# Kernel tuning notes

Measured on AMD Instinct MI355X. Metric: run time of the kernel, lower is better.

Reference implementation:

```python
import jax, jax.numpy as jnp
import numpy as np

B, S, D_IN = 2, 2048, 2048
H, G, HD = 16, 4, 128          # heads, kv groups, head_dim
GS = H // G                    # group size (heads per kv group)
EPS = 1e-6
SCALE = HD ** -0.5


def rms_norm(x, w):
    # RMSNorm over last dim (head_dim)
    var = jnp.mean(jnp.square(x), axis=-1, keepdims=True)
    return x * jax.lax.rsqrt(var + EPS) * w


def apply_rope(x, cos, sin):
    # x: [b, h, s, d]; cos/sin: [s, d]. Rotate-half convention.
    d = x.shape[-1]
    x1, x2 = x[..., : d // 2], x[..., d // 2 :]
    rotated = jnp.concatenate([-x2, x1], axis=-1)
    return x * cos[None, None] + rotated * sin[None, None]


def setup_inputs() -> dict:
    key = jax.random.key(0)
    ks = jax.random.split(key, 8)
    x = jax.random.normal(ks[0], (B, S, D_IN), jnp.float32)
    mask = jnp.triu(jnp.ones((S, S), jnp.bool_), k=1)  # True = masked (future)
    # realistic RoPE tables
    inv_freq = 1.0 / (10000.0 ** (jnp.arange(0, HD, 2, dtype=jnp.float32) / HD))
    angles = jnp.arange(S, dtype=jnp.float32)[:, None] * inv_freq[None, :]  # [S, HD/2]
    angles = jnp.concatenate([angles, angles], axis=-1)  # [S, HD]
    cos, sin = jnp.cos(angles), jnp.sin(angles)
    sd = 0.02
    Wq = jax.random.normal(ks[1], (D_IN, H * HD), jnp.float32) * sd
    Wk = jax.random.normal(ks[2], (D_IN, G * HD), jnp.float32) * sd
    Wv = jax.random.normal(ks[3], (D_IN, G * HD), jnp.float32) * sd
    Wo = jax.random.normal(ks[4], (H * HD, D_IN), jnp.float32) * sd
    q_norm_w = jnp.ones((HD,), jnp.float32)
    k_norm_w = jnp.ones((HD,), jnp.float32)
    return {"x": x, "mask": mask, "cos": cos, "sin": sin, "Wq": Wq, "Wk": Wk,
            "Wv": Wv, "Wo": Wo, "q_norm_w": q_norm_w, "k_norm_w": k_norm_w}


def reference(x, mask, cos, sin, Wq, Wk, Wv, Wo, q_norm_w, k_norm_w):
    b, s, _ = x.shape
    q = (x @ Wq).reshape(b, s, H, HD).transpose(0, 2, 1, 3)   # [b,H,s,d]
    k = (x @ Wk).reshape(b, s, G, HD).transpose(0, 2, 1, 3)   # [b,G,s,d]
    v = (x @ Wv).reshape(b, s, G, HD).transpose(0, 2, 1, 3)   # [b,G,s,d]
    q = rms_norm(q, q_norm_w)
    k = rms_norm(k, k_norm_w)
    q = apply_rope(q, cos, sin)
    k = apply_rope(k, cos, sin)
    q = q * SCALE
    # GQA without materializing repeated KV: split heads into [G, GS]
    qg = q.reshape(b, G, GS, s, HD)                           # [b,G,gs,s,d]
    scores = jnp.einsum('bghsd,bgtd->bghst', qg, k)           # [b,G,gs,s,s]
    scores = jnp.where(mask[None, None, None], -jnp.inf, scores)
    attn = jax.nn.softmax(scores, axis=-1)
    ctx = jnp.einsum('bghst,bgtd->bghsd', attn, v)            # [b,G,gs,s,d]
    ctx = ctx.reshape(b, H, s, HD).transpose(0, 2, 1, 3).reshape(b, s, H * HD)
    return ctx @ Wo
```

## Files before the change

kernel.cpp:

```cpp
#include <hip/hip_runtime.h>
#include <cstdint>
#include <cstddef>

typedef unsigned short u16;
typedef __bf16 bf16x8 __attribute__((ext_vector_type(8)));
typedef float f32x4 __attribute__((ext_vector_type(4)));

#define SLEN 2048
#define NHEADS 16
#define NGRP 4

__device__ inline float bf2f(u16 u) { return __uint_as_float(((unsigned)u) << 16); }
__device__ inline u16 f2bf(float f) {
    unsigned u = __float_as_uint(f);
    u += 0x7fffu + ((u >> 16) & 1u);
    return (u16)(u >> 16);
}

__device__ inline f32x4 mfma16(bf16x8 a, bf16x8 b, f32x4 c) {
    return __builtin_amdgcn_mfma_f32_16x16x32_bf16(a, b, c, 0, 0, 0);
}

__device__ inline void memfence_compiler() { __asm__ volatile("" ::: "memory"); }

__device__ inline void cp16(const u16* g, u16* l) {
    __builtin_amdgcn_global_load_lds(
        (__attribute__((address_space(1))) void*)(u16*)g,
        (__attribute__((address_space(3))) void*)l, 16, 0, 0);
}


__device__ inline void transpose_f32_body(u16 (*tile)[65], const float* __restrict__ in,
                                          u16* __restrict__ out, int R, int C, int bx, int by,
                                          int tid) {
    const long r0 = (long)by * 64, c0 = (long)bx * 64;
    for (int j = 0; j < 4; j++) {
        int c = j * 256 + tid;
        int lr = c >> 4, lc = (c & 15) * 4;
        float4 v = *(const float4*)&in[(r0 + lr) * (long)C + c0 + lc];
        tile[lr][lc + 0] = f2bf(v.x); tile[lr][lc + 1] = f2bf(v.y);
        tile[lr][lc + 2] = f2bf(v.z); tile[lr][lc + 3] = f2bf(v.w);
    }
    __syncthreads();
    for (int j = 0; j < 4; j++) {
        int c = j * 256 + tid;
        int orow = c >> 4, oc = (c & 15) * 4;
        ushort4 vv;
        vv.x = tile[oc + 0][orow]; vv.y = tile[oc + 1][orow];
        vv.z = tile[oc + 2][orow]; vv.w = tile[oc + 3][orow];
        *(ushort4*)&out[(c0 + orow) * (long)R + r0 + oc] = vv;
    }
}

__device__ inline void transpose_bf_body(u16 (*tile)[65], const u16* __restrict__ in, long inRS,
                                         u16* __restrict__ out, int R, int C, int bx, int by,
                                         int tid) {
    const long r0 = (long)by * 64, c0 = (long)bx * 64;
    for (int j = 0; j < 4; j++) {
        int c = j * 256 + tid;
        int lr = c >> 4, lc = (c & 15) * 4;
        ushort4 vv = *(const ushort4*)&in[(r0 + lr) * inRS + c0 + lc];
        tile[lr][lc + 0] = vv.x; tile[lr][lc + 1] = vv.y;
        tile[lr][lc + 2] = vv.z; tile[lr][lc + 3] = vv.w;
    }
    __syncthreads();
    for (int j = 0; j < 4; j++) {
        int c = j * 256 + tid;
        int orow = c >> 4, oc = (c & 15) * 4;
        ushort4 vv;
        vv.x = tile[oc + 0][orow]; vv.y = tile[oc + 1][orow];
        vv.z = tile[oc + 2][orow]; vv.w = tile[oc + 3][orow];
        *(ushort4*)&out[(c0 + orow) * (long)R + r0 + oc] = vv;
    }
}

__device__ inline void normrope_body(u16* __restrict__ buf, long rowstride, int heads,
                                     const u16* __restrict__ w,
                                     const float* __restrict__ cosf, const float* __restrict__ sinf,
                                     float scale, int row, int lane) {
    u16* p = buf + (long)(row / heads) * rowstride + (row % heads) * 128;
    float x1 = bf2f(p[lane]);
    float x2 = bf2f(p[lane + 64]);
    float ss = x1 * x1 + x2 * x2;
    for (int off = 1; off < 64; off <<= 1) ss += __shfl_xor(ss, off);
    float inv = rsqrtf(ss * (1.f / 128.f) + 1e-6f);
    int s = (row / heads) % SLEN;
    float c1 = cosf[s * 128 + lane], c2 = cosf[s * 128 + 64 + lane];
    float s1 = sinf[s * 128 + lane], s2 = sinf[s * 128 + 64 + lane];
    float w1 = bf2f(w[lane]), w2 = bf2f(w[lane + 64]);
    float y1 = x1 * inv * w1, y2 = x2 * inv * w2;
    p[lane]      = f2bf((y1 * c1 - y2 * s1) * scale);
    p[lane + 64] = f2bf((y2 * c2 + y1 * s2) * scale);
}

__global__ __launch_bounds__(256) void prep_k(const float* __restrict__ x, u16* __restrict__ xbf,
                                              const float* __restrict__ qw, const float* __restrict__ kw,
                                              u16* qwb, u16* kwb,
                                              const float* __restrict__ Wq, const float* __restrict__ Wk,
                                              const float* __restrict__ Wv, u16* __restrict__ wqkvT) {
    __shared__ u16 tile[64][65];
    const int bid = blockIdx.x, tid = threadIdx.x;
    if (bid < 8192) {
        long i = ((long)bid * 256 + tid) * 4;
        float4 v = *(const float4*)(x + i);
        ushort4 o;
        o.x = f2bf(v.x); o.y = f2bf(v.y); o.z = f2bf(v.z); o.w = f2bf(v.w);
        *(ushort4*)(xbf + i) = o;
    } else if (bid == 8192) {
        if (tid < 128) qwb[tid] = f2bf(qw[tid]);
        else kwb[tid - 128] = f2bf(kw[tid - 128]);
    } else if (bid < 9217) {
        int rem = bid - 8193;
        transpose_f32_body(tile, Wq, wqkvT, 2048, 2048, rem & 31, rem >> 5, tid);
    } else if (bid < 9473) {
        int rem = bid - 9217;
        transpose_f32_body(tile, Wk, wqkvT + 2048L * 2048, 2048, 512, rem & 7, rem >> 3, tid);
    } else {
        int rem = bid - 9473;
        transpose_f32_body(tile, Wv, wqkvT + 2560L * 2048, 2048, 512, rem & 7, rem >> 3, tid);
    }
}

__global__ __launch_bounds__(256) void mid_k(u16* __restrict__ qkvb, u16* __restrict__ vTb,
                                             const u16* __restrict__ qwb, const u16* __restrict__ kwb,
                                             const float* __restrict__ cosf, const float* __restrict__ sinf,
                                             const float* __restrict__ Wo, u16* __restrict__ woT) {
    __shared__ u16 tile[64][65];
    const int bid = blockIdx.x, tid = threadIdx.x;
    if (bid < 512) {
        transpose_bf_body(tile, qkvb + 2560, 3072L, vTb, 4096, 512, bid & 7, bid >> 3, tid);
    } else if (bid < 16896) {
        int row = (bid - 512) * 4 + (tid >> 6);
        normrope_body(qkvb, 3072L, NHEADS, qwb, cosf, sinf, 0.08838834764831845f, row, tid & 63);
    } else if (bid < 20992) {
        int row = (bid - 16896) * 4 + (tid >> 6);
        normrope_body(qkvb + 2048, 3072L, NGRP, kwb, cosf, sinf, 1.0f, row, tid & 63);
    } else {
        int rem = bid - 20992;
        transpose_f32_body(tile, Wo, woT, 2048, 2048, rem & 31, rem >> 5, tid);
    }
}

template <typename OutT, int NI>
__global__ __launch_bounds__(512, 2) void gemm8p(const u16* __restrict__ A, const u16* __restrict__ Bt,
                                                 OutT* __restrict__ C, int N, int K) {
    extern __shared__ u16 smem[];
    constexpr int AUNIT = 8192;
    constexpr int BUNIT = NI * 2048;
    constexpr int GATE = 2 + NI / 2;
    const int tid = threadIdx.x;
    const int lane = tid & 63, wave = tid >> 6;
    const int l15 = lane & 15, quad = lane >> 4;
    const int wm = (wave >> 2) * 128, wn = (wave & 3) * (NI * 16);
    const long m0 = (long)blockIdx.y * 256, n0 = (long)blockIdx.x * (NI * 64);

    f32x4 acc[8][NI];
    #pragma unroll
    for (int i = 0; i < 8; i++)
        #pragma unroll
        for (int j = 0; j < NI; j++) acc[i][j] = {0.f, 0.f, 0.f, 0.f};

    const u16* aBase = A + m0 * (long)K;
    const u16* bBase = Bt + n0 * (long)K;

    auto stageA = [&](int kt, int c, int k) {
        u16* dst = smem + (c * 2 + k) * AUNIT + wave * 512;
        #pragma unroll
        for (int i = 0; i < 2; i++) {
            int cd = i * 512 + wave * 64 + lane;
            int r = cd >> 2;
            int js = (cd & 3) ^ ((r >> 1) & 3);
            cp16(aBase + (long)r * K + kt + k * 32 + js * 8, dst + i * 4096);
        }
    };
    auto stageB = [&](int kt, int c, int k) {
        u16* dst = smem + 4 * AUNIT + (c * 2 + k) * BUNIT + wave * 512;
        #pragma unroll
        for (int i = 0; i < NI / 2; i++) {
            int cd = i * 512 + wave * 64 + lane;
            int r = cd >> 2;
            int js = (cd & 3) ^ ((r >> 1) & 3);
            cp16(bBase + (long)r * K + kt + k * 32 + js * 8, dst + i * 4096);
        }
    };

    stageA(0, 0, 0); stageB(0, 0, 0); stageA(0, 0, 1); stageB(0, 0, 1);

    const int nkt = K >> 6;

    for (int t = 0; t < nkt; ++t) {
        const int c = t & 1;
        const int kt1 = (t + 1) << 6;
        const bool more = (t + 1) < nkt;
        #pragma unroll
        for (int k = 0; k < 2; ++k) {
            if (k == 0 || more) {
                if constexpr (NI == 4) asm volatile("s_waitcnt vmcnt(4)" ::: "memory");
                else                   asm volatile("s_waitcnt vmcnt(3)" ::: "memory");
            } else {
                asm volatile("s_waitcnt vmcnt(0)" ::: "memory");
            }
            __builtin_amdgcn_s_barrier();

            const u16* au = smem + (c * 2 + k) * AUNIT;
            const u16* bu = smem + 4 * AUNIT + (c * 2 + k) * BUNIT;

            bf16x8 bfr[NI], af[4];
            #pragma unroll
            for (int ni = 0; ni < NI; ni++) {
                const int r = wn + ni * 16 + l15;
                bfr[ni] = *(const bf16x8*)&bu[r * 32 + (quad ^ ((r >> 1) & 3)) * 8];
            }
            #pragma unroll
            for (int mi = 0; mi < 4; mi++) {
                const int r = wm + mi * 16 + l15;
                af[mi] = *(const bf16x8*)&au[r * 32 + (quad ^ ((r >> 1) & 3)) * 8];
            }
            if (more) stageA(kt1, c ^ 1, k);
            asm volatile("s_waitcnt lgkmcnt(0)" ::: "memory");
            __builtin_amdgcn_sched_barrier(0);
            __builtin_amdgcn_s_setprio(1);
            #pragma unroll
            for (int mi = 0; mi < 4; mi++)
                #pragma unroll
                for (int ni = 0; ni < NI; ni++)
                    acc[mi][ni] = mfma16(af[mi], bfr[ni], acc[mi][ni]);
            __builtin_amdgcn_s_setprio(0);
            __builtin_amdgcn_s_barrier();

            #pragma unroll
            for (int mi = 0; mi < 4; mi++) {
                const int r = wm + 64 + mi * 16 + l15;
                af[mi] = *(const bf16x8*)&au[r * 32 + (quad ^ ((r >> 1) & 3)) * 8];
            }
            if (more) stageB(kt1, c ^ 1, k);
            asm volatile("s_waitcnt lgkmcnt(0)" ::: "memory");
            __builtin_amdgcn_sched_barrier(0);
            __builtin_amdgcn_s_setprio(1);
            #pragma unroll
            for (int mi = 0; mi < 4; mi++)
                #pragma unroll
                for (int ni = 0; ni < NI; ni++)
                    acc[4 + mi][ni] = mfma16(af[mi], bfr[ni], acc[4 + mi][ni]);
            __builtin_amdgcn_s_setprio(0);
            __builtin_amdgcn_s_barrier();
        }
    }

    #pragma unroll
    for (int mi = 0; mi < 8; mi++)
        #pragma unroll
        for (int r = 0; r < 4; r++) {
            long row = m0 + wm + mi * 16 + quad * 4 + r;
            OutT* crow = C + row * (long)N + n0 + wn + l15;
            #pragma unroll
            for (int ni = 0; ni < NI; ni++) {
                float v = acc[mi][ni][r];
                if constexpr (sizeof(OutT) == 2) crow[ni * 16] = f2bf(v);
                else crow[ni * 16] = v;
            }
        }
}

__global__ __launch_bounds__(256, 2) void attn(const u16* __restrict__ qkv, const u16* __restrict__ vT,
                                               u16* __restrict__ ctx) {
    __shared__ u16 KB[64 * 128];
    __shared__ u16 VB[128 * 64];
    __shared__ u16 Ps[4][2][16][72];
    __shared__ float Al[4][2][16];
    const int tid = threadIdx.x;
    const int lane = tid & 63, wave = tid >> 6;
    const int l15 = lane & 15, quad = lane >> 4;
    const int bg = blockIdx.x & 7, b = bg >> 2, g = bg & 3;
    const int rest = blockIdx.x >> 3;
    const int h = g * 4 + (rest & 3);
    const int idx = rest >> 2;
    const int qt = (idx < 8) ? (15 - idx) : (idx - 8);
    const int wr = qt * 128 + wave * 32;

    union { bf16x8 v; u16 s[8]; } uo;
    for (int j = 0; j < 8; j++) uo.s[j] = 0x3F80;
    const bf16x8 ones = uo.v;

    bf16x8 qa[2][4];
    for (int m = 0; m < 2; m++) {
        const u16* qp = qkv + (long)(b * SLEN + wr + m * 16 + l15) * 3072 + h * 128 + quad * 8;
        for (int kc = 0; kc < 4; kc++) qa[m][kc] = *(const bf16x8*)(qp + kc * 32);
    }
    float m_i[2] = {-__builtin_inff(), -__builtin_inff()};
    f32x4 l_acc[2];
    f32x4 o[2][8];
    for (int m = 0; m < 2; m++) l_acc[m] = {0.f, 0.f, 0.f, 0.f};
    for (int m = 0; m < 2; m++)
        for (int nf = 0; nf < 8; nf++) o[m][nf] = {0.f, 0.f, 0.f, 0.f};

    const u16* kqb = qkv + (long)b * SLEN * 3072 + 2048 + g * 128;
    const u16* vgb = vT + (long)g * 128 * 4096 + (long)b * SLEN;
    const int xk = (l15 & 7) << 4;
    const int nt = 2 * qt + 2;

    for (int t = 0; t < nt; ++t) {
        const int t0 = t * 64;
        #pragma unroll
        for (int i = 0; i < 4; ++i) {
            const int j = wave * 4 + i;
            {
                const int row = j * 4 + (lane >> 4);
                const int cs = lane & 15;
                cp16(kqb + (long)(t0 + row) * 3072 + ((cs ^ (row & 7)) * 8), &KB[j * 512]);
            }
            {
                const int row = j * 8 + (lane >> 3);
                const int cs = lane & 7;
                cp16(vgb + (long)row * 4096 + t0 + ((cs ^ (row & 7)) * 8), &VB[j * 512]);
            }
        }
        __syncthreads();

        if (t0 <= wr + 31) {
            bf16x8 kf[4][4];
            #pragma unroll
            for (int nf = 0; nf < 4; nf++)
                #pragma unroll
                for (int kc = 0; kc < 4; kc++)
                    kf[nf][kc] = *(const bf16x8*)((const char*)KB +
                                  (nf * 16 + l15) * 256 + ((quad * 16 + kc * 64) ^ xk));

            f32x4 sc[2][4];
            for (int m = 0; m < 2; m++)
                for (int nf = 0; nf < 4; nf++) sc[m][nf] = {0.f, 0.f, 0.f, 0.f};
            #pragma unroll
            for (int kc = 0; kc < 4; kc++)
                #pragma unroll
                for (int nf = 0; nf < 4; nf++) {
                    sc[0][nf] = mfma16(kf[nf][kc], qa[0][kc], sc[0][nf]);
                    sc[1][nf] = mfma16(kf[nf][kc], qa[1][kc], sc[1][nf]);
                }
            if (t0 + 63 > wr) {
                #pragma unroll
                for (int m = 0; m < 2; m++) {
                    int qrow = wr + m * 16 + l15;
                    #pragma unroll
                    for (int nf = 0; nf < 4; nf++)
                        #pragma unroll
                        for (int r = 0; r < 4; r++)
                            if (t0 + nf * 16 + quad * 4 + r > qrow) sc[m][nf][r] = -__builtin_inff();
                }
            }
            float alpha[2];
            #pragma unroll
            for (int m = 0; m < 2; m++) {
                float mx = sc[m][0][0];
                #pragma unroll
                for (int nf = 0; nf < 4; nf++)
                    #pragma unroll
                    for (int r = 0; r < 4; r++) mx = fmaxf(mx, sc[m][nf][r]);
                mx = fmaxf(mx, __shfl_xor(mx, 16));
                mx = fmaxf(mx, __shfl_xor(mx, 32));
                float mn = fmaxf(m_i[m], mx);
                alpha[m] = __expf(m_i[m] - mn);
                m_i[m] = mn;
                Al[wave][m][l15] = alpha[m];
            }
            #pragma unroll
            for (int m = 0; m < 2; m++)
                #pragma unroll
                for (int nf = 0; nf < 4; nf++) {
                    ushort4 pk;
                    pk.x = f2bf(__expf(sc[m][nf][0] - m_i[m]));
                    pk.y = f2bf(__expf(sc[m][nf][1] - m_i[m]));
                    pk.z = f2bf(__expf(sc[m][nf][2] - m_i[m]));
                    pk.w = f2bf(__expf(sc[m][nf][3] - m_i[m]));
                    *(ushort4*)&Ps[wave][m][l15][nf * 16 + quad * 4] = pk;
                }
            memfence_compiler();
            f32x4 al[2];
            al[0] = *(const f32x4*)&Al[wave][0][quad * 4];
            al[1] = *(const f32x4*)&Al[wave][1][quad * 4];
            #pragma unroll
            for (int m = 0; m < 2; m++) {
                #pragma unroll
                for (int nf = 0; nf < 8; nf++)
                    #pragma unroll
                    for (int r = 0; r < 4; r++) o[m][nf][r] *= al[m][r];
                #pragma unroll
                for (int r = 0; r < 4; r++) l_acc[m][r] *= al[m][r];
            }
            {
                bf16x8 vf[8];
                #pragma unroll
                for (int nf = 0; nf < 8; nf++)
                    vf[nf] = *(const bf16x8*)((const char*)VB +
                              (nf * 16 + l15) * 128 + ((quad * 16) ^ xk));
                bf16x8 pa0 = *(const bf16x8*)&Ps[wave][0][l15][quad * 8];
                bf16x8 pa1 = *(const bf16x8*)&Ps[wave][1][l15][quad * 8];
                #pragma unroll
                for (int nf = 0; nf < 8; nf++) {
                    o[0][nf] = mfma16(pa0, vf[nf], o[0][nf]);
                    o[1][nf] = mfma16(pa1, vf[nf], o[1][nf]);
                }
                l_acc[0] = mfma16(pa0, ones, l_acc[0]);
                l_acc[1] = mfma16(pa1, ones, l_acc[1]);
            }
            {
                bf16x8 vf[8];
                #pragma unroll
                for (int nf = 0; nf < 8; nf++)
                    vf[nf] = *(const bf16x8*)((const char*)VB +
                              (nf * 16 + l15) * 128 + ((64 + quad * 16) ^ xk));
                bf16x8 pa0 = *(const bf16x8*)&Ps[wave][0][l15][32 + quad * 8];
                bf16x8 pa1 = *(const bf16x8*)&Ps[wave][1][l15][32 + quad * 8];
                #pragma unroll
                for (int nf = 0; nf < 8; nf++) {
                    o[0][nf] = mfma16(pa0, vf[nf], o[0][nf]);
                    o[1][nf] = mfma16(pa1, vf[nf], o[1][nf]);
                }
                l_acc[0] = mfma16(pa0, ones, l_acc[0]);
                l_acc[1] = mfma16(pa1, ones, l_acc[1]);
            }
            memfence_compiler();
        }
        __syncthreads();
    }

    #pragma unroll
    for (int m = 0; m < 2; m++)
        #pragma unroll
        for (int r = 0; r < 4; r++) {
            float inv = 1.f / l_acc[m][r];
            int srow = wr + m * 16 + quad * 4 + r;
            u16* cp = ctx + (long)(b * SLEN + srow) * 2048 + h * 128 + l15;
            #pragma unroll
            for (int nf = 0; nf < 8; nf++) cp[nf * 16] = f2bf(o[m][nf][r] * inv);
        }
}

extern "C" void kernel_launch(void* const* d_in, const int* in_sizes, int n_in,
                              void* d_out, int out_size, void* d_ws, size_t ws_size,
                              hipStream_t stream) {
    const float* x    = (const float*)d_in[0];
    const float* cosi = (const float*)d_in[2];
    const float* sini = (const float*)d_in[3];
    const float* Wq   = (const float*)d_in[4];
    const float* Wk   = (const float*)d_in[5];
    const float* Wv   = (const float*)d_in[6];
    const float* Wo   = (const float*)d_in[7];
    const float* qw   = (const float*)d_in[8];
    const float* kw   = (const float*)d_in[9];
    float* out = (float*)d_out;
    char* ws = (char*)d_ws;

    const size_t MB = 1 << 20;
    u16* qkvb  = (u16*)(ws);
    u16* vTb   = (u16*)(ws + 24 * MB);
    u16* xbf   = (u16*)(ws + 28 * MB);
    u16* ctx   = (u16*)(ws + 28 * MB);
    u16* wqkvT = (u16*)(ws + 44 * MB);
    u16* woT   = (u16*)(ws + 44 * MB);
    u16* qwb   = (u16*)(ws + 56 * MB);
    u16* kwb   = (u16*)(ws + 56 * MB + 256);

    prep_k<<<9729, 256, 0, stream>>>(x, xbf, qw, kw, qwb, kwb, Wq, Wk, Wv, wqkvT);

    gemm8p<u16, 4><<<dim3(12, 16), 512, 131072, stream>>>(xbf, wqkvT, qkvb, 3072, 2048);

    mid_k<<<22016, 256, 0, stream>>>(qkvb, vTb, qwb, kwb, cosi, sini, Wo, woT);

    attn<<<dim3(512, 1, 1), 256, 0, stream>>>(qkvb, vTb, ctx);

    gemm8p<float, 2><<<dim3(16, 16), 512, 98304, stream>>>(ctx, woT, out, 2048, 2048);
}
```

Baseline: 320.2 us.

## Double-buffer attention K/V tiles, hoist V fragments, swizzle GEMM block order

The attention kernel now double-buffers the K and V shared tiles. It prefetches the next tile with async copies while computing on the current one, and uses a partial vmcnt wait instead of a full sync. V fragments are loaded once per tile, and the P staging buffer is cut to one row-block per wave, reused across the two m iterations. In the GEMM, both A fragment halves are loaded up front with a partial lgkmcnt wait, and block indices are remapped in an XCD-aware interleave to improve L2 locality. The changes cost more LDS and registers, which may hurt occupancy, and they rely on exact async-copy counts and per-wave buffer reuse being ordered correctly.

```diff
diff --git a/kernel.cpp b/kernel.cpp
--- a/kernel.cpp
+++ b/kernel.cpp
@@ -147,12 +147,16 @@
     extern __shared__ u16 smem[];
     constexpr int AUNIT = 8192;
     constexpr int BUNIT = NI * 2048;
-    constexpr int GATE = 2 + NI / 2;
     const int tid = threadIdx.x;
     const int lane = tid & 63, wave = tid >> 6;
     const int l15 = lane & 15, quad = lane >> 4;
     const int wm = (wave >> 2) * 128, wn = (wave & 3) * (NI * 16);
-    const long m0 = (long)blockIdx.y * 256, n0 = (long)blockIdx.x * (NI * 64);
+
+    const int nbx = gridDim.x;
+    const int nwg = nbx * gridDim.y;
+    const int d = blockIdx.y * nbx + blockIdx.x;
+    const int s = (d & 7) * (nwg >> 3) + (d >> 3);
+    const long m0 = (long)(s / nbx) * 256, n0 = (long)(s % nbx) * (NI * 64);
 
     f32x4 acc[8][NI];
     #pragma unroll
@@ -205,7 +209,7 @@
             const u16* au = smem + (c * 2 + k) * AUNIT;
             const u16* bu = smem + 4 * AUNIT + (c * 2 + k) * BUNIT;
 
-            bf16x8 bfr[NI], af[4];
+            bf16x8 bfr[NI], af0[4], af1[4];
             #pragma unroll
             for (int ni = 0; ni < NI; ni++) {
                 const int r = wn + ni * 16 + l15;
@@ -214,25 +218,25 @@
             #pragma unroll
             for (int mi = 0; mi < 4; mi++) {
                 const int r = wm + mi * 16 + l15;
-                af[mi] = *(const bf16x8*)&au[r * 32 + (quad ^ ((r >> 1) & 3)) * 8];
+                af0[mi] = *(const bf16x8*)&au[r * 32 + (quad ^ ((r >> 1) & 3)) * 8];
+            }
+            #pragma unroll
+            for (int mi = 0; mi < 4; mi++) {
+                const int r = wm + 64 + mi * 16 + l15;
+                af1[mi] = *(const bf16x8*)&au[r * 32 + (quad ^ ((r >> 1) & 3)) * 8];
             }
             if (more) stageA(kt1, c ^ 1, k);
-            asm volatile("s_waitcnt lgkmcnt(0)" ::: "memory");
+            asm volatile("s_waitcnt lgkmcnt(4)" ::: "memory");
             __builtin_amdgcn_sched_barrier(0);
             __builtin_amdgcn_s_setprio(1);
             #pragma unroll
             for (int mi = 0; mi < 4; mi++)
                 #pragma unroll
                 for (int ni = 0; ni < NI; ni++)
-                    acc[mi][ni] = mfma16(af[mi], bfr[ni], acc[mi][ni]);
+                    acc[mi][ni] = mfma16(af0[mi], bfr[ni], acc[mi][ni]);
             __builtin_amdgcn_s_setprio(0);
             __builtin_amdgcn_s_barrier();
 
-            #pragma unroll
-            for (int mi = 0; mi < 4; mi++) {
-                const int r = wm + 64 + mi * 16 + l15;
-                af[mi] = *(const bf16x8*)&au[r * 32 + (quad ^ ((r >> 1) & 3)) * 8];
-            }
             if (more) stageB(kt1, c ^ 1, k);
             asm volatile("s_waitcnt lgkmcnt(0)" ::: "memory");
             __builtin_amdgcn_sched_barrier(0);
@@ -241,7 +245,7 @@
             for (int mi = 0; mi < 4; mi++)
                 #pragma unroll
                 for (int ni = 0; ni < NI; ni++)
-                    acc[4 + mi][ni] = mfma16(af[mi], bfr[ni], acc[4 + mi][ni]);
+                    acc[4 + mi][ni] = mfma16(af1[mi], bfr[ni], acc[4 + mi][ni]);
             __builtin_amdgcn_s_setprio(0);
             __builtin_amdgcn_s_barrier();
         }
@@ -264,9 +268,9 @@
 
 __global__ __launch_bounds__(256, 2) void attn(const u16* __restrict__ qkv, const u16* __restrict__ vT,
                                                u16* __restrict__ ctx) {
-    __shared__ u16 KB[64 * 128];
-    __shared__ u16 VB[128 * 64];
-    __shared__ u16 Ps[4][2][16][72];
+    __shared__ u16 KB[2][64 * 128];
+    __shared__ u16 VB[2][128 * 64];
+    __shared__ u16 Ps[4][16][72];
     __shared__ float Al[4][2][16];
     const int tid = threadIdx.x;
     const int lane = tid & 63, wave = tid >> 6;
@@ -299,23 +303,35 @@
     const int xk = (l15 & 7) << 4;
     const int nt = 2 * qt + 2;
 
-    for (int t = 0; t < nt; ++t) {
-        const int t0 = t * 64;
+    auto stage = [&](int t0, int buf) {
         #pragma unroll
         for (int i = 0; i < 4; ++i) {
             const int j = wave * 4 + i;
             {
                 const int row = j * 4 + (lane >> 4);
                 const int cs = lane & 15;
-                cp16(kqb + (long)(t0 + row) * 3072 + ((cs ^ (row & 7)) * 8), &KB[j * 512]);
+                cp16(kqb + (long)(t0 + row) * 3072 + ((cs ^ (row & 7)) * 8), &KB[buf][j * 512]);
             }
             {
                 const int row = j * 8 + (lane >> 3);
                 const int cs = lane & 7;
-                cp16(vgb + (long)row * 4096 + t0 + ((cs ^ (row & 7)) * 8), &VB[j * 512]);
-            }
-        }
-        __syncthreads();
+                cp16(vgb + (long)row * 4096 + t0 + ((cs ^ (row & 7)) * 8), &VB[buf][j * 512]);
+            }
+        }
+    };
+
+    stage(0, 0);
+
+    for (int t = 0; t < nt; ++t) {
+        const int cur = t & 1;
+        const int t0 = t * 64;
+        if (t + 1 < nt) {
+            stage((t + 1) * 64, cur ^ 1);
+            asm volatile("s_waitcnt vmcnt(8)" ::: "memory");
+        } else {
+            asm volatile("s_waitcnt vmcnt(0)" ::: "memory");
+        }
+        __builtin_amdgcn_s_barrier();
 
         if (t0 <= wr + 31) {
             bf16x8 kf[4][4];
@@ -323,7 +339,7 @@
             for (int nf = 0; nf < 4; nf++)
                 #pragma unroll
                 for (int kc = 0; kc < 4; kc++)
-                    kf[nf][kc] = *(const bf16x8*)((const char*)KB +
+                    kf[nf][kc] = *(const bf16x8*)((const char*)&KB[cur][0] +
                                   (nf * 16 + l15) * 256 + ((quad * 16 + kc * 64) ^ xk));
 
             f32x4 sc[2][4];
@@ -362,8 +378,22 @@
                 m_i[m] = mn;
                 Al[wave][m][l15] = alpha[m];
             }
-            #pragma unroll
-            for (int m = 0; m < 2; m++)
+            memfence_compiler();
+            f32x4 al[2];
+            al[0] = *(const f32x4*)&Al[wave][0][quad * 4];
+            al[1] = *(const f32x4*)&Al[wave][1][quad * 4];
+
+            bf16x8 vfA[8], vfB[8];
+            #pragma unroll
+            for (int nf = 0; nf < 8; nf++) {
+                vfA[nf] = *(const bf16x8*)((const char*)&VB[cur][0] +
+                          (nf * 16 + l15) * 128 + ((quad * 16) ^ xk));
+                vfB[nf] = *(const bf16x8*)((const char*)&VB[cur][0] +
+                          (nf * 16 + l15) * 128 + ((64 + quad * 16) ^ xk));
+            }
+
+            #pragma unroll
+            for (int m = 0; m < 2; m++) {
                 #pragma unroll
                 for (int nf = 0; nf < 4; nf++) {
                     ushort4 pk;
@@ -371,56 +401,29 @@
                     pk.y = f2bf(__expf(sc[m][nf][1] - m_i[m]));
                     pk.z = f2bf(__expf(sc[m][nf][2] - m_i[m]));
                     pk.w = f2bf(__expf(sc[m][nf][3] - m_i[m]));
-                    *(ushort4*)&Ps[wave][m][l15][nf * 16 + quad * 4] = pk;
+                    *(ushort4*)&Ps[wave][l15][nf * 16 + quad * 4] = pk;
                 }
-            memfence_compiler();
-            f32x4 al[2];
-            al[0] = *(const f32x4*)&Al[wave][0][quad * 4];
-            al[1] = *(const f32x4*)&Al[wave][1][quad * 4];
-            #pragma unroll
-            for (int m = 0; m < 2; m++) {
+                memfence_compiler();
                 #pragma unroll
                 for (int nf = 0; nf < 8; nf++)
                     #pragma unroll
                     for (int r = 0; r < 4; r++) o[m][nf][r] *= al[m][r];
                 #pragma unroll
                 for (int r = 0; r < 4; r++) l_acc[m][r] *= al[m][r];
-            }
-            {
-                bf16x8 vf[8];
-                #pragma unroll
-                for (int nf = 0; nf < 8; nf++)
-                    vf[nf] = *(const bf16x8*)((const char*)VB +
-                              (nf * 16 + l15) * 128 + ((quad * 16) ^ xk));
-                bf16x8 pa0 = *(const bf16x8*)&Ps[wave][0][l15][quad * 8];
-                bf16x8 pa1 = *(const bf16x8*)&Ps[wave][1][l15][quad * 8];
+                bf16x8 pa0 = *(const bf16x8*)&Ps[wave][l15][quad * 8];
+                bf16x8 pa1 = *(const bf16x8*)&Ps[wave][l15][32 + quad * 8];
                 #pragma unroll
                 for (int nf = 0; nf < 8; nf++) {
-                    o[0][nf] = mfma16(pa0, vf[nf], o[0][nf]);
-                    o[1][nf] = mfma16(pa1, vf[nf], o[1][nf]);
+                    o[m][nf] = mfma16(pa0, vfA[nf], o[m][nf]);
+                    o[m][nf] = mfma16(pa1, vfB[nf], o[m][nf]);
                 }
-                l_acc[0] = mfma16(pa0, ones, l_acc[0]);
-                l_acc[1] = mfma16(pa1, ones, l_acc[1]);
-            }
-            {
-                bf16x8 vf[8];
-                #pragma unroll
-                for (int nf = 0; nf < 8; nf++)
-                    vf[nf] = *(const bf16x8*)((const char*)VB +
-                              (nf * 16 + l15) * 128 + ((64 + quad * 16) ^ xk));
-                bf16x8 pa0 = *(const bf16x8*)&Ps[wave][0][l15][32 + quad * 8];
-                bf16x8 pa1 = *(const bf16x8*)&Ps[wave][1][l15][32 + quad * 8];
-                #pragma unroll
-                for (int nf = 0; nf < 8; nf++) {
-                    o[0][nf] = mfma16(pa0, vf[nf], o[0][nf]);
-                    o[1][nf] = mfma16(pa1, vf[nf], o[1][nf]);
-                }
-                l_acc[0] = mfma16(pa0, ones, l_acc[0]);
-                l_acc[1] = mfma16(pa1, ones, l_acc[1]);
-            }
-            memfence_compiler();
-        }
-        __syncthreads();
+                l_acc[m] = mfma16(pa0, ones, l_acc[m]);
+                l_acc[m] = mfma16(pa1, ones, l_acc[m]);
+                memfence_compiler();
+            }
+        }
+        memfence_compiler();
+        __builtin_amdgcn_s_barrier();
     }
 
     #pragma unroll
```

Result: no change. 315.0 us (-1.6%).

## Split long causal attention tiles across blocks with flag-synchronized merge, remap GEMM blocks

Applied to the files above, without the earlier changes.

The attention kernel now uses a static schedule table. Each block handles up to two query tiles, and the longest query tiles are split across two blocks by KV range. The block that owns the first half writes its partial output plus row max and row sum, then raises a flag; the second block spin-waits on that flag and merges the two halves using log-sum-exp rescaling. The aim is to balance the causal triangle's uneven work across the 512 blocks. Separately, the GEMM remaps block IDs across groups of 8 for better cache locality and loads both A-fragment halves before the first MFMA batch. The spin-wait relies on the producer block being resident or already finished, which risks deadlock or stalls if scheduling order differs.

```diff
diff --git a/kernel.cpp b/kernel.cpp
--- a/kernel.cpp
+++ b/kernel.cpp
@@ -124,7 +124,8 @@
 __global__ __launch_bounds__(256) void mid_k(u16* __restrict__ qkvb, u16* __restrict__ vTb,
                                              const u16* __restrict__ qwb, const u16* __restrict__ kwb,
                                              const float* __restrict__ cosf, const float* __restrict__ sinf,
-                                             const float* __restrict__ Wo, u16* __restrict__ woT) {
+                                             const float* __restrict__ Wo, u16* __restrict__ woT,
+                                             unsigned* __restrict__ flags) {
     __shared__ u16 tile[64][65];
     const int bid = blockIdx.x, tid = threadIdx.x;
     if (bid < 512) {
@@ -135,9 +136,11 @@
     } else if (bid < 20992) {
         int row = (bid - 16896) * 4 + (tid >> 6);
         normrope_body(qkvb + 2048, 3072L, NGRP, kwb, cosf, sinf, 1.0f, row, tid & 63);
-    } else {
+    } else if (bid < 22016) {
         int rem = bid - 20992;
         transpose_f32_body(tile, Wo, woT, 2048, 2048, rem & 31, rem >> 5, tid);
+    } else {
+        flags[tid] = 0u;
     }
 }
 
@@ -147,12 +150,16 @@
     extern __shared__ u16 smem[];
     constexpr int AUNIT = 8192;
     constexpr int BUNIT = NI * 2048;
-    constexpr int GATE = 2 + NI / 2;
     const int tid = threadIdx.x;
     const int lane = tid & 63, wave = tid >> 6;
     const int l15 = lane & 15, quad = lane >> 4;
     const int wm = (wave >> 2) * 128, wn = (wave & 3) * (NI * 16);
-    const long m0 = (long)blockIdx.y * 256, n0 = (long)blockIdx.x * (NI * 64);
+
+    const int nbx = gridDim.x;
+    const int nwg = nbx * gridDim.y;
+    const int d = blockIdx.y * nbx + blockIdx.x;
+    const int s = (d & 7) * (nwg >> 3) + (d >> 3);
+    const long m0 = (long)(s / nbx) * 256, n0 = (long)(s % nbx) * (NI * 64);
 
     f32x4 acc[8][NI];
     #pragma unroll
@@ -205,7 +212,7 @@
             const u16* au = smem + (c * 2 + k) * AUNIT;
             const u16* bu = smem + 4 * AUNIT + (c * 2 + k) * BUNIT;
 
-            bf16x8 bfr[NI], af[4];
+            bf16x8 bfr[NI], af0[4], af1[4];
             #pragma unroll
             for (int ni = 0; ni < NI; ni++) {
                 const int r = wn + ni * 16 + l15;
@@ -214,25 +221,25 @@
             #pragma unroll
             for (int mi = 0; mi < 4; mi++) {
                 const int r = wm + mi * 16 + l15;
-                af[mi] = *(const bf16x8*)&au[r * 32 + (quad ^ ((r >> 1) & 3)) * 8];
+                af0[mi] = *(const bf16x8*)&au[r * 32 + (quad ^ ((r >> 1) & 3)) * 8];
+            }
+            #pragma unroll
+            for (int mi = 0; mi < 4; mi++) {
+                const int r = wm + 64 + mi * 16 + l15;
+                af1[mi] = *(const bf16x8*)&au[r * 32 + (quad ^ ((r >> 1) & 3)) * 8];
             }
             if (more) stageA(kt1, c ^ 1, k);
-            asm volatile("s_waitcnt lgkmcnt(0)" ::: "memory");
+            asm volatile("s_waitcnt lgkmcnt(4)" ::: "memory");
             __builtin_amdgcn_sched_barrier(0);
             __builtin_amdgcn_s_setprio(1);
             #pragma unroll
             for (int mi = 0; mi < 4; mi++)
                 #pragma unroll
                 for (int ni = 0; ni < NI; ni++)
-                    acc[mi][ni] = mfma16(af[mi], bfr[ni], acc[mi][ni]);
+                    acc[mi][ni] = mfma16(af0[mi], bfr[ni], acc[mi][ni]);
             __builtin_amdgcn_s_setprio(0);
             __builtin_amdgcn_s_barrier();
 
-            #pragma unroll
-            for (int mi = 0; mi < 4; mi++) {
-                const int r = wm + 64 + mi * 16 + l15;
-                af[mi] = *(const bf16x8*)&au[r * 32 + (quad ^ ((r >> 1) & 3)) * 8];
-            }
             if (more) stageB(kt1, c ^ 1, k);
             asm volatile("s_waitcnt lgkmcnt(0)" ::: "memory");
             __builtin_amdgcn_sched_barrier(0);
@@ -241,7 +248,7 @@
             for (int mi = 0; mi < 4; mi++)
                 #pragma unroll
                 for (int ni = 0; ni < NI; ni++)
-                    acc[4 + mi][ni] = mfma16(af[mi], bfr[ni], acc[4 + mi][ni]);
+                    acc[4 + mi][ni] = mfma16(af1[mi], bfr[ni], acc[4 + mi][ni]);
             __builtin_amdgcn_s_setprio(0);
             __builtin_amdgcn_s_barrier();
         }
@@ -263,7 +270,9 @@
 }
 
 __global__ __launch_bounds__(256, 2) void attn(const u16* __restrict__ qkv, const u16* __restrict__ vT,
-                                               u16* __restrict__ ctx) {
+                                               u16* __restrict__ ctx,
+                                               float* __restrict__ mlm, float* __restrict__ mll,
+                                               unsigned* __restrict__ flags) {
     __shared__ u16 KB[64 * 128];
     __shared__ u16 VB[128 * 64];
     __shared__ u16 Ps[4][2][16][72];
@@ -273,166 +282,228 @@
     const int l15 = lane & 15, quad = lane >> 4;
     const int bg = blockIdx.x & 7, b = bg >> 2, g = bg & 3;
     const int rest = blockIdx.x >> 3;
-    const int h = g * 4 + (rest & 3);
-    const int idx = rest >> 2;
-    const int qt = (idx < 8) ? (15 - idx) : (idx - 8);
-    const int wr = qt * 128 + wave * 32;
+    const int hh = rest & 3, h = g * 4 + hh;
+    const int slot = rest >> 2;
+
+    unsigned long long W;
+    if (slot < 4)       W = 0x003E002E003F002FULL;
+    else if (slot < 8)  W = 0x003C002C003D002DULL;
+    else if (slot < 12) W = 0x393A292A383B282BULL;
+    else                W = 0x1314121511161017ULL;
+    const unsigned ent = (unsigned)(W >> ((slot & 3) * 16)) & 0xFFFFu;
 
     union { bf16x8 v; u16 s[8]; } uo;
     for (int j = 0; j < 8; j++) uo.s[j] = 0x3F80;
     const bf16x8 ones = uo.v;
 
-    bf16x8 qa[2][4];
-    for (int m = 0; m < 2; m++) {
-        const u16* qp = qkv + (long)(b * SLEN + wr + m * 16 + l15) * 3072 + h * 128 + quad * 8;
-        for (int kc = 0; kc < 4; kc++) qa[m][kc] = *(const bf16x8*)(qp + kc * 32);
-    }
-    float m_i[2] = {-__builtin_inff(), -__builtin_inff()};
-    f32x4 l_acc[2];
-    f32x4 o[2][8];
-    for (int m = 0; m < 2; m++) l_acc[m] = {0.f, 0.f, 0.f, 0.f};
-    for (int m = 0; m < 2; m++)
-        for (int nf = 0; nf < 8; nf++) o[m][nf] = {0.f, 0.f, 0.f, 0.f};
-
     const u16* kqb = qkv + (long)b * SLEN * 3072 + 2048 + g * 128;
     const u16* vgb = vT + (long)g * 128 * 4096 + (long)b * SLEN;
     const int xk = (l15 & 7) << 4;
-    const int nt = 2 * qt + 2;
-
-    for (int t = 0; t < nt; ++t) {
-        const int t0 = t * 64;
-        #pragma unroll
-        for (int i = 0; i < 4; ++i) {
-            const int j = wave * 4 + i;
-            {
-                const int row = j * 4 + (lane >> 4);
-                const int cs = lane & 15;
-                cp16(kqb + (long)(t0 + row) * 3072 + ((cs ^ (row & 7)) * 8), &KB[j * 512]);
-            }
-            {
-                const int row = j * 8 + (lane >> 3);
-                const int cs = lane & 7;
-                cp16(vgb + (long)row * 4096 + t0 + ((cs ^ (row & 7)) * 8), &VB[j * 512]);
-            }
-        }
-        __syncthreads();
-
-        if (t0 <= wr + 31) {
-            bf16x8 kf[4][4];
-            #pragma unroll
-            for (int nf = 0; nf < 4; nf++)
+
+    for (int tk = 0; tk < 2; ++tk) {
+        const unsigned e = tk ? (ent >> 8) : ent;
+        const int qt = e & 15, md = (e >> 4) & 3;
+        if (md == 0) break;
+        const int wr = qt * 128 + wave * 32;
+        const int sig = (bg * 4 + hh) * 8 + (qt - 8);
+        const int tbeg = (md == 3) ? (qt + 1) : 0;
+        const int tend = (md == 2) ? (qt + 1) : (2 * qt + 2);
+
+        bf16x8 qa[2][4];
+        for (int m = 0; m < 2; m++) {
+            const u16* qp = qkv + (long)(b * SLEN + wr + m * 16 + l15) * 3072 + h * 128 + quad * 8;
+            for (int kc = 0; kc < 4; kc++) qa[m][kc] = *(const bf16x8*)(qp + kc * 32);
+        }
+        float m_i[2] = {-__builtin_inff(), -__builtin_inff()};
+        f32x4 l_acc[2];
+        f32x4 o[2][8];
+        for (int m = 0; m < 2; m++) l_acc[m] = {0.f, 0.f, 0.f, 0.f};
+        for (int m = 0; m < 2; m++)
+            for (int nf = 0; nf < 8; nf++) o[m][nf] = {0.f, 0.f, 0.f, 0.f};
+
+        for (int t = tbeg; t < tend; ++t) {
+            const int t0 = t * 64;
+            #pragma unroll
+            for (int i = 0; i < 4; ++i) {
+                const int j = wave * 4 + i;
+                {
+                    const int row = j * 4 + (lane >> 4);
+                    const int cs = lane & 15;
+                    cp16(kqb + (long)(t0 + row) * 3072 + ((cs ^ (row & 7)) * 8), &KB[j * 512]);
+                }
+                {
+                    const int row = j * 8 + (lane >> 3);
+                    const int cs = lane & 7;
+                    cp16(vgb + (long)row * 4096 + t0 + ((cs ^ (row & 7)) * 8), &VB[j * 512]);
+                }
+            }
+            __syncthreads();
+
+            if (t0 <= wr + 31) {
+                bf16x8 kf[4][4];
+                #pragma unroll
+                for (int nf = 0; nf < 4; nf++)
+                    #pragma unroll
+                    for (int kc = 0; kc < 4; kc++)
+                        kf[nf][kc] = *(const bf16x8*)((const char*)KB +
+                                      (nf * 16 + l15) * 256 + ((quad * 16 + kc * 64) ^ xk));
+
+                f32x4 sc[2][4];
+                for (int m = 0; m < 2; m++)
+                    for (int nf = 0; nf < 4; nf++) sc[m][nf] = {0.f, 0.f, 0.f, 0.f};
                 #pragma unroll
                 for (int kc = 0; kc < 4; kc++)
-                    kf[nf][kc] = *(const bf16x8*)((const char*)KB +
-                                  (nf * 16 + l15) * 256 + ((quad * 16 + kc * 64) ^ xk));
-
-            f32x4 sc[2][4];
-            for (int m = 0; m < 2; m++)
-                for (int nf = 0; nf < 4; nf++) sc[m][nf] = {0.f, 0.f, 0.f, 0.f};
-            #pragma unroll
-            for (int kc = 0; kc < 4; kc++)
-                #pragma unroll
-                for (int nf = 0; nf < 4; nf++) {
-                    sc[0][nf] = mfma16(kf[nf][kc], qa[0][kc], sc[0][nf]);
-                    sc[1][nf] = mfma16(kf[nf][kc], qa[1][kc], sc[1][nf]);
-                }
-            if (t0 + 63 > wr) {
+                    #pragma unroll
+                    for (int nf = 0; nf < 4; nf++) {
+                        sc[0][nf] = mfma16(kf[nf][kc], qa[0][kc], sc[0][nf]);
+                        sc[1][nf] = mfma16(kf[nf][kc], qa[1][kc], sc[1][nf]);
+                    }
+                if (t0 + 63 > wr) {
+                    #pragma unroll
+                    for (int m = 0; m < 2; m++) {
+                        int qrow = wr + m * 16 + l15;
+                        #pragma unroll
+                        for (int nf = 0; nf < 4; nf++)
+                            #pragma unroll
+                            for (int r = 0; r < 4; r++)
+                                if (t0 + nf * 16 + quad * 4 + r > qrow) sc[m][nf][r] = -__builtin_inff();
+                    }
+                }
+                float alpha[2];
                 #pragma unroll
                 for (int m = 0; m < 2; m++) {
-                    int qrow = wr + m * 16 + l15;
+                    float mx = sc[m][0][0];
                     #pragma unroll
                     for (int nf = 0; nf < 4; nf++)
                         #pragma unroll
+                        for (int r = 0; r < 4; r++) mx = fmaxf(mx, sc[m][nf][r]);
+                    mx = fmaxf(mx, __shfl_xor(mx, 16));
+                    mx = fmaxf(mx, __shfl_xor(mx, 32));
+                    float mn = fmaxf(m_i[m], mx);
+                    alpha[m] = __expf(m_i[m] - mn);
+                    m_i[m] = mn;
+                    Al[wave][m][l15] = alpha[m];
+                }
+                #pragma unroll
+                for (int m = 0; m < 2; m++)
+                    #pragma unroll
+                    for (int nf = 0; nf < 4; nf++) {
+                        ushort4 pk;
+                        pk.x = f2bf(__expf(sc[m][nf][0] - m_i[m]));
+                        pk.y = f2bf(__expf(sc[m][nf][1] - m_i[m]));
+                        pk.z = f2bf(__expf(sc[m][nf][2] - m_i[m]));
+                        pk.w = f2bf(__expf(sc[m][nf][3] - m_i[m]));
+                        *(ushort4*)&Ps[wave][m][l15][nf * 16 + quad * 4] = pk;
+                    }
+                memfence_compiler();
+                f32x4 al[2];
+                al[0] = *(const f32x4*)&Al[wave][0][quad * 4];
+                al[1] = *(const f32x4*)&Al[wave][1][quad * 4];
+                #pragma unroll
+                for (int m = 0; m < 2; m++) {
+                    #pragma unroll
+                    for (int nf = 0; nf < 8; nf++)
+                        #pragma unroll
+                        for (int r = 0; r < 4; r++) o[m][nf][r] *= al[m][r];
+                    #pragma unroll
+                    for (int r = 0; r < 4; r++) l_acc[m][r] *= al[m][r];
+                }
+                {
+                    bf16x8 vf[8];
+                    #pragma unroll
+                    for (int nf = 0; nf < 8; nf++)
+                        vf[nf] = *(const bf16x8*)((const char*)VB +
+                                  (nf * 16 + l15) * 128 + ((quad * 16) ^ xk));
+                    bf16x8 pa0 = *(const bf16x8*)&Ps[wave][0][l15][quad * 8];
+                    bf16x8 pa1 = *(const bf16x8*)&Ps[wave][1][l15][quad * 8];
+                    #pragma unroll
+                    for (int nf = 0; nf < 8; nf++) {
+                        o[0][nf] = mfma16(pa0, vf[nf], o[0][nf]);
+                        o[1][nf] = mfma16(pa1, vf[nf], o[1][nf]);
+                    }
+                    l_acc[0] = mfma16(pa0, ones, l_acc[0]);
+                    l_acc[1] = mfma16(pa1, ones, l_acc[1]);
+                }
+                {
+                    bf16x8 vf[8];
+                    #pragma unroll
+                    for (int nf = 0; nf < 8; nf++)
+                        vf[nf] = *(const bf16x8*)((const char*)VB +
+                                  (nf * 16 + l15) * 128 + ((64 + quad * 16) ^ xk));
+                    bf16x8 pa0 = *(const bf16x8*)&Ps[wave][0][l15][32 + quad * 8];
+                    bf16x8 pa1 = *(const bf16x8*)&Ps[wave][1][l15][32 + quad * 8];
+                    #pragma unroll
+                    for (int nf = 0; nf < 8; nf++) {
+                        o[0][nf] = mfma16(pa0, vf[nf], o[0][nf]);
+                        o[1][nf] = mfma16(pa1, vf[nf], o[1][nf]);
+                    }
+                    l_acc[0] = mfma16(pa0, ones, l_acc[0]);
+                    l_acc[1] = mfma16(pa1, ones, l_acc[1]);
+                }
+                memfence_compiler();
+            }
+            __syncthreads();
+        }
+
+        if (md != 3) {
+            #pragma unroll
+            for (int m = 0; m < 2; m++)
+                #pragma unroll
+                for (int r = 0; r < 4; r++) {
+                    float inv = 1.f / l_acc[m][r];
+                    int srow = wr + m * 16 + quad * 4 + r;
+                    u16* cp = ctx + (long)(b * SLEN + srow) * 2048 + h * 128 + l15;
+                    #pragma unroll
+                    for (int nf = 0; nf < 8; nf++) cp[nf * 16] = f2bf(o[m][nf][r] * inv);
+                }
+            if (md == 2) {
+                #pragma unroll
+                for (int m = 0; m < 2; m++) {
+                    if (quad == 0) mlm[sig * 128 + wave * 32 + m * 16 + l15] = m_i[m];
+                    if (l15 == 0) {
+                        #pragma unroll
                         for (int r = 0; r < 4; r++)
-                            if (t0 + nf * 16 + quad * 4 + r > qrow) sc[m][nf][r] = -__builtin_inff();
-                }
-            }
-            float alpha[2];
-            #pragma unroll
-            for (int m = 0; m < 2; m++) {
-                float mx = sc[m][0][0];
-                #pragma unroll
-                for (int nf = 0; nf < 4; nf++)
-                    #pragma unroll
-                    for (int r = 0; r < 4; r++) mx = fmaxf(mx, sc[m][nf][r]);
-                mx = fmaxf(mx, __shfl_xor(mx, 16));
-                mx = fmaxf(mx, __shfl_xor(mx, 32));
-                float mn = fmaxf(m_i[m], mx);
-                alpha[m] = __expf(m_i[m] - mn);
-                m_i[m] = mn;
-                Al[wave][m][l15] = alpha[m];
-            }
+                            mll[sig * 128 + wave * 32 + m * 16 + quad * 4 + r] = l_acc[m][r];
+                    }
+                }
+                __threadfence();
+                __syncthreads();
+                if (tid == 0) atomicExch(&flags[sig], 1u);
+            }
+        } else {
+            Al[wave][0][l15] = m_i[0];
+            Al[wave][1][l15] = m_i[1];
+            memfence_compiler();
+            if (tid == 0) {
+                while (atomicAdd(&flags[sig], 0u) == 0u) { __builtin_amdgcn_s_sleep(8); }
+            }
+            __syncthreads();
+            __threadfence();
+            f32x4 mB[2];
+            mB[0] = *(const f32x4*)&Al[wave][0][quad * 4];
+            mB[1] = *(const f32x4*)&Al[wave][1][quad * 4];
             #pragma unroll
             for (int m = 0; m < 2; m++)
                 #pragma unroll
-                for (int nf = 0; nf < 4; nf++) {
-                    ushort4 pk;
-                    pk.x = f2bf(__expf(sc[m][nf][0] - m_i[m]));
-                    pk.y = f2bf(__expf(sc[m][nf][1] - m_i[m]));
-                    pk.z = f2bf(__expf(sc[m][nf][2] - m_i[m]));
-                    pk.w = f2bf(__expf(sc[m][nf][3] - m_i[m]));
-                    *(ushort4*)&Ps[wave][m][l15][nf * 16 + quad * 4] = pk;
-                }
-            memfence_compiler();
-            f32x4 al[2];
-            al[0] = *(const f32x4*)&Al[wave][0][quad * 4];
-            al[1] = *(const f32x4*)&Al[wave][1][quad * 4];
-            #pragma unroll
-            for (int m = 0; m < 2; m++) {
-                #pragma unroll
-                for (int nf = 0; nf < 8; nf++)
-                    #pragma unroll
-                    for (int r = 0; r < 4; r++) o[m][nf][r] *= al[m][r];
-                #pragma unroll
-                for (int r = 0; r < 4; r++) l_acc[m][r] *= al[m][r];
-            }
-            {
-                bf16x8 vf[8];
-                #pragma unroll
-                for (int nf = 0; nf < 8; nf++)
-                    vf[nf] = *(const bf16x8*)((const char*)VB +
-                              (nf * 16 + l15) * 128 + ((quad * 16) ^ xk));
-                bf16x8 pa0 = *(const bf16x8*)&Ps[wave][0][l15][quad * 8];
-                bf16x8 pa1 = *(const bf16x8*)&Ps[wave][1][l15][quad * 8];
-                #pragma unroll
-                for (int nf = 0; nf < 8; nf++) {
-                    o[0][nf] = mfma16(pa0, vf[nf], o[0][nf]);
-                    o[1][nf] = mfma16(pa1, vf[nf], o[1][nf]);
-                }
-                l_acc[0] = mfma16(pa0, ones, l_acc[0]);
-                l_acc[1] = mfma16(pa1, ones, l_acc[1]);
-            }
-            {
-                bf16x8 vf[8];
-                #pragma unroll
-                for (int nf = 0; nf < 8; nf++)
-                    vf[nf] = *(const bf16x8*)((const char*)VB +
-                              (nf * 16 + l15) * 128 + ((64 + quad * 16) ^ xk));
-                bf16x8 pa0 = *(const bf16x8*)&Ps[wave][0][l15][32 + quad * 8];
-                bf16x8 pa1 = *(const bf16x8*)&Ps[wave][1][l15][32 + quad * 8];
-                #pragma unroll
-                for (int nf = 0; nf < 8; nf++) {
-                    o[0][nf] = mfma16(pa0, vf[nf], o[0][nf]);
-                    o[1][nf] = mfma16(pa1, vf[nf], o[1][nf]);
-                }
-                l_acc[0] = mfma16(pa0, ones, l_acc[0]);
-                l_acc[1] = mfma16(pa1, ones, l_acc[1]);
-            }
-            memfence_compiler();
+                for (int r = 0; r < 4; r++) {
+                    int rl = wave * 32 + m * 16 + quad * 4 + r;
+                    float mA = mlm[sig * 128 + rl];
+                    float lA = mll[sig * 128 + rl];
+                    float M  = fmaxf(mA, mB[m][r]);
+                    float wA = lA * __expf(mA - M);
+                    float eB = __expf(mB[m][r] - M);
+                    float invd = 1.f / (wA + l_acc[m][r] * eB);
+                    int srow = wr + m * 16 + quad * 4 + r;
+                    u16* cp = ctx + (long)(b * SLEN + srow) * 2048 + h * 128 + l15;
+                    #pragma unroll
+                    for (int nf = 0; nf < 8; nf++) {
+                        float oA = bf2f(cp[nf * 16]);
+                        cp[nf * 16] = f2bf((wA * oA + eB * o[m][nf][r]) * invd);
+                    }
+                }
         }
         __syncthreads();
     }
-
-    #pragma unroll
-    for (int m = 0; m < 2; m++)
-        #pragma unroll
-        for (int r = 0; r < 4; r++) {
-            float inv = 1.f / l_acc[m][r];
-            int srow = wr + m * 16 + quad * 4 + r;
-            u16* cp = ctx + (long)(b * SLEN + srow) * 2048 + h * 128 + l15;
-            #pragma unroll
-            for (int nf = 0; nf < 8; nf++) cp[nf * 16] = f2bf(o[m][nf][r] * inv);
-        }
 }
 
 extern "C" void kernel_launch(void* const* d_in, const int* in_sizes, int n_in,
@@ -459,14 +530,17 @@
     u16* woT   = (u16*)(ws + 44 * MB);
     u16* qwb   = (u16*)(ws + 56 * MB);
     u16* kwb   = (u16*)(ws + 56 * MB + 256);
+    float* mlm = (float*)(ws + 57 * MB);
+    float* mll = (float*)(ws + 57 * MB + 128 * 1024);
+    unsigned* flags = (unsigned*)(ws + 57 * MB + 256 * 1024);
 
     prep_k<<<9729, 256, 0, stream>>>(x, xbf, qw, kw, qwb, kwb, Wq, Wk, Wv, wqkvT);
 
     gemm8p<u16, 4><<<dim3(12, 16), 512, 131072, stream>>>(xbf, wqkvT, qkvb, 3072, 2048);
 
-    mid_k<<<22016, 256, 0, stream>>>(qkvb, vTb, qwb, kwb, cosi, sini, Wo, woT);
-
-    attn<<<dim3(512, 1, 1), 256, 0, stream>>>(qkvb, vTb, ctx);
+    mid_k<<<22017, 256, 0, stream>>>(qkvb, vTb, qwb, kwb, cosi, sini, Wo, woT, flags);
+
+    attn<<<dim3(512, 1, 1), 256, 0, stream>>>(qkvb, vTb, ctx, mlm, mll, flags);
 
     gemm8p<float, 2><<<dim3(16, 16), 512, 98304, stream>>>(ctx, woT, out, 2048, 2048);
 }
```

Measured after the change: 368.9 us. 15.2% more time.
